# Kernel tuning notes

Hardware: AMD Instinct MI355X
Metric: run time of the kernel (lower is better)

The kernel has to match this reference:

```python
import jax, jax.numpy as jnp
import numpy as np

EMBED_DIM = 1024
LATEN_DIM = 1024
B, S = 4, 2048


def setup_inputs() -> dict:
    key = jax.random.key(0)
    k1, k2, k3, k4, k5 = jax.random.split(key, 5)
    xq = jax.random.normal(k1, (B, S, EMBED_DIM), dtype=jnp.float32)
    xk = jax.random.normal(k2, (B, S, EMBED_DIM), dtype=jnp.float32)
    xv = jax.random.normal(k3, (B, S, EMBED_DIM), dtype=jnp.float32)
    # Linear weight init similar to torch default scale
    bound = 1.0 / np.sqrt(EMBED_DIM)
    Wq = jax.random.uniform(k4, (EMBED_DIM, EMBED_DIM), minval=-bound, maxval=bound, dtype=jnp.float32)
    bq = jax.random.uniform(k5, (EMBED_DIM,), minval=-bound, maxval=bound, dtype=jnp.float32)
    # causal mask: 1 => masked (future positions)
    att_mask = jnp.triu(jnp.ones((S, S), dtype=jnp.int32), k=1)
    return {"xq": xq, "xk": xk, "xv": xv, "Wq": Wq, "bq": bq, "att_mask": att_mask}


def reference(xq, xk, xv, Wq, bq, att_mask):
    scale = LATEN_DIM ** (-0.5)
    # Faithful to source: linearQ is applied to all three inputs.
    Q = jnp.einsum('bsd,ed->bse', xq, Wq) + bq
    K = jnp.einsum('bsd,ed->bse', xk, Wq) + bq
    V = jnp.einsum('bsd,ed->bse', xv, Wq) + bq
    scores = jnp.einsum('bqe,bke->bqk', Q, K) * scale  # [B, S, S]
    scores = jnp.where(att_mask == 1, -jnp.inf, scores)
    probs = jax.nn.softmax(scores, axis=-1)
    return jnp.einsum('bqk,bke->bqe', probs, V)
```

## Files before the change

kernel.cpp:

```cpp
#include <hip/hip_runtime.h>
#include <hip/hip_bf16.h>
#include <stdint.h>


typedef __attribute__((ext_vector_type(8))) short bf16x8;
typedef __attribute__((ext_vector_type(4))) float floatx4;

#define DEVI static __device__ __forceinline__

static constexpr int S_ = 2048;
static constexpr int E_ = 1024;
static constexpr int BATCH = 4;
static constexpr int N4X = 8192 * 1024 / 4;

DEVI unsigned short f2b(float f) {
  union { float f; unsigned u; } v; v.f = f;
  return (unsigned short)((v.u + 0x7FFFu + ((v.u >> 16) & 1u)) >> 16);
}

DEVI void async_load16(const void* g, void* l) {
  __builtin_amdgcn_global_load_lds(
      (__attribute__((address_space(1))) void*)(void*)(g),
      (__attribute__((address_space(3))) void*)(l),
      16, 0, 0);
}

DEVI void mfma_tile(const unsigned short* lsA, const unsigned short* lsB,
                    int m0, int n0, int lrow, int lk, floatx4 (&acc)[4][4]) {
  bf16x8 af[4], bfr[4];
#pragma unroll
  for (int i = 0; i < 4; ++i)
    af[i] = *(const bf16x8*)(lsA + (m0 + i * 16 + lrow) * 32 + lk);
#pragma unroll
  for (int i = 0; i < 4; ++i)
    bfr[i] = *(const bf16x8*)(lsB + (n0 + i * 16 + lrow) * 32 + lk);
#pragma unroll
  for (int mi = 0; mi < 4; ++mi)
#pragma unroll
    for (int ni = 0; ni < 4; ++ni)
      acc[mi][ni] = __builtin_amdgcn_mfma_f32_16x16x32_bf16(
          af[mi], bfr[ni], acc[mi][ni], 0, 0, 0);
}

DEVI void stage_bf16(const unsigned short* src, unsigned short* ls, int ld,
                     int tid) {
#pragma unroll
  for (int j = 0; j < 2; ++j) {
    int t = tid + j * 256, row = t >> 2, kk = (t & 3) << 3;
    async_load16(src + (size_t)row * ld + kk, ls + t * 8);
  }
}

__global__ void cvt_all(const float* __restrict__ xq,
                        const float* __restrict__ xk,
                        const float* __restrict__ xv,
                        const float* __restrict__ Wq,
                        unsigned short* __restrict__ Xb,
                        unsigned short* __restrict__ Wb) {
  int i = blockIdx.x * blockDim.x + threadIdx.x;
  const float4* src;
  ushort4* dst;
  if (i < 3 * N4X) {
    int seg = i / N4X, off = i - seg * N4X;
    const float* s = (seg == 0) ? xq : (seg == 1) ? xk : xv;
    src = (const float4*)s + off;
    dst = (ushort4*)(Xb + (size_t)seg * 8192 * 1024) + off;
  } else {
    int off = i - 3 * N4X;
    src = (const float4*)Wq + off;
    dst = (ushort4*)Wb + off;
  }
  float4 v = *src;
  ushort4 o;
  o.x = f2b(v.x); o.y = f2b(v.y); o.z = f2b(v.z); o.w = f2b(v.w);
  *dst = o;
}

__global__ __launch_bounds__(256) void gemm_qkv(
    const unsigned short* __restrict__ Xb, const unsigned short* __restrict__ Wb,
    const float* __restrict__ bias, unsigned short* __restrict__ Qb,
    unsigned short* __restrict__ Kb, unsigned short* __restrict__ Vt) {
  __shared__ __align__(16) unsigned short lsA[2][128 * 32];
  __shared__ __align__(16) unsigned short lsB[2][128 * 32];
  const int l = blockIdx.x;
  const int xcd = l & 7, i = l >> 3;
  const int bn = i & 7;
  const int bmg = xcd * 24 + (i >> 3);
  const int input = bmg / 64, bm = bmg % 64;
  const unsigned short* A = Xb + (size_t)bmg * 128 * 1024;
  const unsigned short* W = Wb + (size_t)bn * 128 * 1024;

  const int tid = threadIdx.x;
  const int lane = tid & 63, wave = tid >> 6;
  const int m0 = (wave >> 1) * 64, n0 = (wave & 1) * 64;
  const int lrow = lane & 15, lk = (lane >> 4) * 8;

  floatx4 acc[4][4] = {};

  for (int kt = 0; kt < 16; ++kt) {
    if (kt) __syncthreads();
    stage_bf16(A + kt * 64, lsA[0], 1024, tid);
    stage_bf16(A + kt * 64 + 32, lsA[1], 1024, tid);
    stage_bf16(W + kt * 64, lsB[0], 1024, tid);
    stage_bf16(W + kt * 64 + 32, lsB[1], 1024, tid);
    __syncthreads();
    mfma_tile(lsA[0], lsB[0], m0, n0, lrow, lk, acc);
    mfma_tile(lsA[1], lsB[1], m0, n0, lrow, lk, acc);
  }

  unsigned short* C = (input == 0) ? Qb : (input == 1) ? Kb : Vt;
  const int rb = (lane >> 4) * 4;
#pragma unroll
  for (int mi = 0; mi < 4; ++mi)
#pragma unroll
    for (int ni = 0; ni < 4; ++ni) {
      int gcol = bn * 128 + n0 + ni * 16 + lrow;
      float bv = bias[gcol];
#pragma unroll
      for (int r = 0; r < 4; ++r) {
        int grow = bm * 128 + m0 + mi * 16 + rb + r;
        unsigned short val = f2b(acc[mi][ni][r] + bv);
        if (input == 2) {
          int b = grow >> 11, s = grow & 2047;
          C[((size_t)b * 1024 + gcol) * 2048 + s] = val;
        } else {
          C[(size_t)grow * 1024 + gcol] = val;
        }
      }
    }
}

__global__ __launch_bounds__(256) void gemm_scores_exp(
    const unsigned short* __restrict__ Qb,
    const unsigned short* __restrict__ Kb, unsigned short* __restrict__ P,
    float* __restrict__ lsum) {
  const int l = blockIdx.x;
  const int xcd = l & 7, k = l >> 3;
  const int m = k & 7, gl = k >> 3;
  const int gg = xcd * 12 + gl;
  const int z = gg / 24, r0 = gg % 24;
  const int bm = (r0 < 8) ? r0 : 8 + ((r0 - 8) >> 1);
  const int bn = ((r0 < 8) ? 0 : ((r0 - 8) & 1)) * 8 + m;
  if (bn > bm) return;

  __shared__ __align__(16) unsigned short lsA[2][128 * 32];
  __shared__ __align__(16) unsigned short lsB[2][128 * 32];
  const unsigned short* A = Qb + ((size_t)z * S_ + bm * 128) * E_;
  const unsigned short* Bt = Kb + ((size_t)z * S_ + bn * 128) * E_;
  const int tid = threadIdx.x;
  const int lane = tid & 63, wave = tid >> 6;
  const int m0 = (wave >> 1) * 64, n0 = (wave & 1) * 64;
  const int lrow = lane & 15, lk = (lane >> 4) * 8;

  floatx4 acc[4][4] = {};
  for (int kt = 0; kt < 16; ++kt) {
    if (kt) __syncthreads();
    stage_bf16(A + kt * 64, lsA[0], E_, tid);
    stage_bf16(A + kt * 64 + 32, lsA[1], E_, tid);
    stage_bf16(Bt + kt * 64, lsB[0], E_, tid);
    stage_bf16(Bt + kt * 64 + 32, lsB[1], E_, tid);
    __syncthreads();
    mfma_tile(lsA[0], lsB[0], m0, n0, lrow, lk, acc);
    mfma_tile(lsA[1], lsB[1], m0, n0, lrow, lk, acc);
  }

  const int rb = (lane >> 4) * 4;
  const bool diag = (bm == bn);
#pragma unroll
  for (int mi = 0; mi < 4; ++mi)
#pragma unroll
    for (int r = 0; r < 4; ++r) {
      const int grow = bm * 128 + m0 + mi * 16 + rb + r;
      float rsum = 0.f;
#pragma unroll
      for (int ni = 0; ni < 4; ++ni) {
        const int gcol = bn * 128 + n0 + ni * 16 + lrow;
        float p = __expf(acc[mi][ni][r] * 0.03125f);
        if (diag && gcol > grow) p = 0.f;
        P[((size_t)z * S_ + grow) * S_ + gcol] = f2b(p);
        rsum += p;
      }
#pragma unroll
      for (int off = 1; off < 16; off <<= 1) rsum += __shfl_xor(rsum, off);
      if ((lane & 15) == 0) atomicAdd(&lsum[z * S_ + grow], rsum);
    }
}

__global__ __launch_bounds__(256) void gemm_pv(
    const unsigned short* __restrict__ Pb,
    const unsigned short* __restrict__ Vt, const float* __restrict__ lsum,
    float* __restrict__ Out) {
  __shared__ __align__(16) unsigned short lsA[2][128 * 32];
  __shared__ __align__(16) unsigned short lsB[2][128 * 32];
  const int l = blockIdx.x;
  const int xcd = l & 7, i = l >> 3;
  const int bn = i & 7, j = i >> 3;
  const int z = j >> 1;
  const int bm = (j & 1) ? xcd : 15 - xcd;

  const unsigned short* A = Pb + ((size_t)z * S_ + bm * 128) * S_;
  const unsigned short* Bt = Vt + ((size_t)z * E_ + bn * 128) * S_;
  float* C = Out + (size_t)z * S_ * E_;
  const int tid = threadIdx.x;
  const int lane = tid & 63, wave = tid >> 6;
  const int m0 = (wave >> 1) * 64, n0 = (wave & 1) * 64;
  const int lrow = lane & 15, lk = (lane >> 4) * 8;

  floatx4 acc[4][4] = {};
  const int nKK = (bm + 1) * 2;
  for (int kt = 0; kt < nKK; ++kt) {
    if (kt) __syncthreads();
    stage_bf16(A + kt * 64, lsA[0], S_, tid);
    stage_bf16(A + kt * 64 + 32, lsA[1], S_, tid);
    stage_bf16(Bt + kt * 64, lsB[0], S_, tid);
    stage_bf16(Bt + kt * 64 + 32, lsB[1], S_, tid);
    __syncthreads();
    mfma_tile(lsA[0], lsB[0], m0, n0, lrow, lk, acc);
    mfma_tile(lsA[1], lsB[1], m0, n0, lrow, lk, acc);
  }

  const int rb = (lane >> 4) * 4;
#pragma unroll
  for (int mi = 0; mi < 4; ++mi)
#pragma unroll
    for (int r = 0; r < 4; ++r) {
      const int grow = bm * 128 + m0 + mi * 16 + rb + r;
      const float inv = 1.0f / lsum[z * S_ + grow];
#pragma unroll
      for (int ni = 0; ni < 4; ++ni) {
        const int gcol = bn * 128 + n0 + ni * 16 + lrow;
        C[(size_t)grow * E_ + gcol] = acc[mi][ni][r] * inv;
      }
    }
}

extern "C" void kernel_launch(void* const* d_in, const int* in_sizes, int n_in,
                              void* d_out, int out_size, void* d_ws,
                              size_t ws_size, hipStream_t stream) {
  (void)in_sizes; (void)n_in; (void)out_size; (void)ws_size;
  const float* xq = (const float*)d_in[0];
  const float* xk = (const float*)d_in[1];
  const float* xv = (const float*)d_in[2];
  const float* Wq = (const float*)d_in[3];
  const float* bq = (const float*)d_in[4];
  float* out = (float*)d_out;

  unsigned short* base16 = (unsigned short*)d_ws;
  unsigned short* Xb = base16;
  unsigned short* P = base16;
  unsigned short* Wb = base16 + (size_t)24 * 1024 * 1024;
  unsigned short* Qb = Wb + (size_t)1024 * 1024;
  unsigned short* Kb = Qb + (size_t)8192 * 1024;
  unsigned short* Vt = Kb + (size_t)8192 * 1024;
  float* lsum = (float*)(Vt + (size_t)8192 * 1024);

  hipMemsetAsync(lsum, 0, BATCH * S_ * sizeof(float), stream);

  const int n4tot = 3 * N4X + 1024 * 1024 / 4;
  cvt_all<<<n4tot / 256, 256, 0, stream>>>(xq, xk, xv, Wq, Xb, Wb);

  gemm_qkv<<<1536, 256, 0, stream>>>(Xb, Wb, bq, Qb, Kb, Vt);
  gemm_scores_exp<<<768, 256, 0, stream>>>(Qb, Kb, P, lsum);
  gemm_pv<<<512, 256, 0, stream>>>(P, Vt, lsum, out);
}
```

Before: 308.3 us.

## Double-buffer GEMM k-loop with swizzled LDS and 512-thread 128x256 tiles

```diff
diff --git a/kernel.cpp b/kernel.cpp
--- a/kernel.cpp
+++ b/kernel.cpp
@@ -25,29 +25,84 @@
       16, 0, 0);
 }
 
-DEVI void mfma_tile(const unsigned short* lsA, const unsigned short* lsB,
-                    int m0, int n0, int lrow, int lk, floatx4 (&acc)[4][4]) {
-  bf16x8 af[4], bfr[4];
-#pragma unroll
-  for (int i = 0; i < 4; ++i)
-    af[i] = *(const bf16x8*)(lsA + (m0 + i * 16 + lrow) * 32 + lk);
-#pragma unroll
-  for (int i = 0; i < 4; ++i)
-    bfr[i] = *(const bf16x8*)(lsB + (n0 + i * 16 + lrow) * 32 + lk);
-#pragma unroll
-  for (int mi = 0; mi < 4; ++mi)
-#pragma unroll
-    for (int ni = 0; ni < 4; ++ni)
-      acc[mi][ni] = __builtin_amdgcn_mfma_f32_16x16x32_bf16(
-          af[mi], bfr[ni], acc[mi][ni], 0, 0, 0);
-}
-
-DEVI void stage_bf16(const unsigned short* src, unsigned short* ls, int ld,
-                     int tid) {
-#pragma unroll
-  for (int j = 0; j < 2; ++j) {
-    int t = tid + j * 256, row = t >> 2, kk = (t & 3) << 3;
-    async_load16(src + (size_t)row * ld + kk, ls + t * 8);
+template <int ROWS>
+DEVI void stage(const unsigned short* __restrict__ src, int ld,
+                unsigned short* ls, int tid) {
+#pragma unroll
+  for (int j = 0; j < ROWS / 64; ++j) {
+    const int u = tid + j * 512;
+    const int row = u >> 3, slot = u & 7;
+    async_load16(src + row * ld + ((slot ^ (row & 7)) << 3), ls + u * 8);
+  }
+}
+
+DEVI bf16x8 ldfrag(const unsigned short* ls, int r, int kslot) {
+  return *(const bf16x8*)(ls + r * 64 + ((kslot ^ (r & 7)) << 3));
+}
+
+template <int NFR>
+DEVI void kloop(const unsigned short* __restrict__ A, int lda,
+                const unsigned short* __restrict__ Bm, int ldb, int NT,
+                unsigned short* lsA, unsigned short* lsB, int tid,
+                floatx4 (&acc)[4][NFR]) {
+  const int lane = tid & 63;
+  const int wr = (tid >> 6) >> 2, wc = (tid >> 6) & 3;
+  const int lrow = lane & 15, g = lane >> 4;
+  constexpr int BROWS = NFR * 64;
+  constexpr int AH = 128 * 64, BH = BROWS * 64;
+
+  stage<128>(A, lda, lsA, tid);
+  stage<BROWS>(Bm, ldb, lsB, tid);
+  if (NT > 1) {
+    stage<128>(A + 64, lda, lsA + AH, tid);
+    stage<BROWS>(Bm + 64, ldb, lsB + BH, tid);
+  }
+
+  for (int t = 0; t < NT; ++t) {
+    const int par = t & 1;
+    if (t + 1 < NT) {
+      if constexpr (NFR == 4)
+        asm volatile("s_waitcnt vmcnt(6)" ::: "memory");
+      else
+        asm volatile("s_waitcnt vmcnt(4)" ::: "memory");
+    } else {
+      asm volatile("s_waitcnt vmcnt(0)" ::: "memory");
+    }
+    asm volatile("s_barrier" ::: "memory");
+
+    const unsigned short* la = lsA + par * AH;
+    const unsigned short* lb = lsB + par * BH;
+    bf16x8 a[4][2];
+#pragma unroll
+    for (int mi = 0; mi < 4; ++mi)
+#pragma unroll
+      for (int ks = 0; ks < 2; ++ks)
+        a[mi][ks] = ldfrag(la, wr * 64 + mi * 16 + lrow, g + ks * 4);
+#pragma unroll
+    for (int nq = 0; nq < NFR / 2; ++nq) {
+      bf16x8 b[2][2];
+#pragma unroll
+      for (int ni = 0; ni < 2; ++ni)
+#pragma unroll
+        for (int ks = 0; ks < 2; ++ks)
+          b[ni][ks] = ldfrag(lb, wc * (NFR * 16) + (nq * 2 + ni) * 16 + lrow,
+                             g + ks * 4);
+      __builtin_amdgcn_s_setprio(1);
+#pragma unroll
+      for (int mi = 0; mi < 4; ++mi)
+#pragma unroll
+        for (int ni = 0; ni < 2; ++ni)
+#pragma unroll
+          for (int ks = 0; ks < 2; ++ks)
+            acc[mi][nq * 2 + ni] = __builtin_amdgcn_mfma_f32_16x16x32_bf16(
+                a[mi][ks], b[ni][ks], acc[mi][nq * 2 + ni], 0, 0, 0);
+      __builtin_amdgcn_s_setprio(0);
+    }
+    asm volatile("s_barrier" ::: "memory");
+    if (t + 2 < NT) {
+      stage<128>(A + (t + 2) * 64, lda, lsA + par * AH, tid);
+      stage<BROWS>(Bm + (t + 2) * 64, ldb, lsB + par * BH, tid);
+    }
   }
 }
 
@@ -76,50 +131,39 @@
   *dst = o;
 }
 
-__global__ __launch_bounds__(256) void gemm_qkv(
+__global__ __launch_bounds__(512) void gemm_qkv(
     const unsigned short* __restrict__ Xb, const unsigned short* __restrict__ Wb,
     const float* __restrict__ bias, unsigned short* __restrict__ Qb,
     unsigned short* __restrict__ Kb, unsigned short* __restrict__ Vt) {
-  __shared__ __align__(16) unsigned short lsA[2][128 * 32];
-  __shared__ __align__(16) unsigned short lsB[2][128 * 32];
+  __shared__ __align__(16) unsigned short lsA[2 * 128 * 64];
+  __shared__ __align__(16) unsigned short lsB[2 * 256 * 64];
   const int l = blockIdx.x;
   const int xcd = l & 7, i = l >> 3;
-  const int bn = i & 7;
-  const int bmg = xcd * 24 + (i >> 3);
-  const int input = bmg / 64, bm = bmg % 64;
+  const int gid = xcd * 96 + i;
+  const int bn = gid & 3, bmg = gid >> 2;
   const unsigned short* A = Xb + (size_t)bmg * 128 * 1024;
-  const unsigned short* W = Wb + (size_t)bn * 128 * 1024;
-
+  const unsigned short* W = Wb + (size_t)bn * 256 * 1024;
   const int tid = threadIdx.x;
+
+  floatx4 acc[4][4] = {};
+  kloop<4>(A, 1024, W, 1024, 16, lsA, lsB, tid, acc);
+
   const int lane = tid & 63, wave = tid >> 6;
-  const int m0 = (wave >> 1) * 64, n0 = (wave & 1) * 64;
-  const int lrow = lane & 15, lk = (lane >> 4) * 8;
-
-  floatx4 acc[4][4] = {};
-
-  for (int kt = 0; kt < 16; ++kt) {
-    if (kt) __syncthreads();
-    stage_bf16(A + kt * 64, lsA[0], 1024, tid);
-    stage_bf16(A + kt * 64 + 32, lsA[1], 1024, tid);
-    stage_bf16(W + kt * 64, lsB[0], 1024, tid);
-    stage_bf16(W + kt * 64 + 32, lsB[1], 1024, tid);
-    __syncthreads();
-    mfma_tile(lsA[0], lsB[0], m0, n0, lrow, lk, acc);
-    mfma_tile(lsA[1], lsB[1], m0, n0, lrow, lk, acc);
-  }
-
+  const int wr = wave >> 2, wc = wave & 3;
+  const int lrow = lane & 15, rb = (lane >> 4) * 4;
+  const int input = bmg >> 6;
   unsigned short* C = (input == 0) ? Qb : (input == 1) ? Kb : Vt;
-  const int rb = (lane >> 4) * 4;
+  const int rowbase = (bmg & 63) * 128 + wr * 64;
 #pragma unroll
   for (int mi = 0; mi < 4; ++mi)
 #pragma unroll
     for (int ni = 0; ni < 4; ++ni) {
-      int gcol = bn * 128 + n0 + ni * 16 + lrow;
-      float bv = bias[gcol];
+      const int gcol = bn * 256 + wc * 64 + ni * 16 + lrow;
+      const float bv = bias[gcol];
 #pragma unroll
       for (int r = 0; r < 4; ++r) {
-        int grow = bm * 128 + m0 + mi * 16 + rb + r;
-        unsigned short val = f2b(acc[mi][ni][r] + bv);
+        const int grow = rowbase + mi * 16 + rb + r;
+        const unsigned short val = f2b(acc[mi][ni][r] + bv);
         if (input == 2) {
           int b = grow >> 11, s = grow & 2047;
           C[((size_t)b * 1024 + gcol) * 2048 + s] = val;
@@ -130,51 +174,41 @@
     }
 }
 
-__global__ __launch_bounds__(256) void gemm_scores_exp(
+__global__ __launch_bounds__(512) void gemm_scores_exp(
     const unsigned short* __restrict__ Qb,
     const unsigned short* __restrict__ Kb, unsigned short* __restrict__ P,
     float* __restrict__ lsum) {
+  __shared__ __align__(16) unsigned short lsA[2 * 128 * 64];
+  __shared__ __align__(16) unsigned short lsB[2 * 256 * 64];
   const int l = blockIdx.x;
-  const int xcd = l & 7, k = l >> 3;
-  const int m = k & 7, gl = k >> 3;
-  const int gg = xcd * 12 + gl;
-  const int z = gg / 24, r0 = gg % 24;
-  const int bm = (r0 < 8) ? r0 : 8 + ((r0 - 8) >> 1);
-  const int bn = ((r0 < 8) ? 0 : ((r0 - 8) & 1)) * 8 + m;
-  if (bn > bm) return;
-
-  __shared__ __align__(16) unsigned short lsA[2][128 * 32];
-  __shared__ __align__(16) unsigned short lsB[2][128 * 32];
+  const int xcd = l & 7, i = l >> 3;
+  const int gid = xcd * 36 + i;
+  const int z = gid / 72;
+  int r0 = gid % 72;
+  int bm = 0;
+  for (;;) { const int c = (bm >> 1) + 1; if (r0 < c) break; r0 -= c; ++bm; }
+  const int bnn = r0;
+
   const unsigned short* A = Qb + ((size_t)z * S_ + bm * 128) * E_;
-  const unsigned short* Bt = Kb + ((size_t)z * S_ + bn * 128) * E_;
+  const unsigned short* Bt = Kb + ((size_t)z * S_ + bnn * 256) * E_;
   const int tid = threadIdx.x;
+
+  floatx4 acc[4][4] = {};
+  kloop<4>(A, E_, Bt, E_, 16, lsA, lsB, tid, acc);
+
   const int lane = tid & 63, wave = tid >> 6;
-  const int m0 = (wave >> 1) * 64, n0 = (wave & 1) * 64;
-  const int lrow = lane & 15, lk = (lane >> 4) * 8;
-
-  floatx4 acc[4][4] = {};
-  for (int kt = 0; kt < 16; ++kt) {
-    if (kt) __syncthreads();
-    stage_bf16(A + kt * 64, lsA[0], E_, tid);
-    stage_bf16(A + kt * 64 + 32, lsA[1], E_, tid);
-    stage_bf16(Bt + kt * 64, lsB[0], E_, tid);
-    stage_bf16(Bt + kt * 64 + 32, lsB[1], E_, tid);
-    __syncthreads();
-    mfma_tile(lsA[0], lsB[0], m0, n0, lrow, lk, acc);
-    mfma_tile(lsA[1], lsB[1], m0, n0, lrow, lk, acc);
-  }
-
-  const int rb = (lane >> 4) * 4;
-  const bool diag = (bm == bn);
+  const int wr = wave >> 2, wc = wave & 3;
+  const int lrow = lane & 15, rb = (lane >> 4) * 4;
+  const bool diag = (bnn == (bm >> 1));
 #pragma unroll
   for (int mi = 0; mi < 4; ++mi)
 #pragma unroll
     for (int r = 0; r < 4; ++r) {
-      const int grow = bm * 128 + m0 + mi * 16 + rb + r;
+      const int grow = bm * 128 + wr * 64 + mi * 16 + rb + r;
       float rsum = 0.f;
 #pragma unroll
       for (int ni = 0; ni < 4; ++ni) {
-        const int gcol = bn * 128 + n0 + ni * 16 + lrow;
+        const int gcol = bnn * 256 + wc * 64 + ni * 16 + lrow;
         float p = __expf(acc[mi][ni][r] * 0.03125f);
         if (diag && gcol > grow) p = 0.f;
         P[((size_t)z * S_ + grow) * S_ + gcol] = f2b(p);
@@ -186,12 +220,12 @@
     }
 }
 
-__global__ __launch_bounds__(256) void gemm_pv(
+__global__ __launch_bounds__(512) void gemm_pv(
     const unsigned short* __restrict__ Pb,
     const unsigned short* __restrict__ Vt, const float* __restrict__ lsum,
     float* __restrict__ Out) {
-  __shared__ __align__(16) unsigned short lsA[2][128 * 32];
-  __shared__ __align__(16) unsigned short lsB[2][128 * 32];
+  __shared__ __align__(16) unsigned short lsA[2 * 128 * 64];
+  __shared__ __align__(16) unsigned short lsB[2 * 128 * 64];
   const int l = blockIdx.x;
   const int xcd = l & 7, i = l >> 3;
   const int bn = i & 7, j = i >> 3;
@@ -202,33 +236,23 @@
   const unsigned short* Bt = Vt + ((size_t)z * E_ + bn * 128) * S_;
   float* C = Out + (size_t)z * S_ * E_;
   const int tid = threadIdx.x;
+  const int NT = 2 * bm + 2;
+
+  floatx4 acc[4][2] = {};
+  kloop<2>(A, S_, Bt, S_, NT, lsA, lsB, tid, acc);
+
   const int lane = tid & 63, wave = tid >> 6;
-  const int m0 = (wave >> 1) * 64, n0 = (wave & 1) * 64;
-  const int lrow = lane & 15, lk = (lane >> 4) * 8;
-
-  floatx4 acc[4][4] = {};
-  const int nKK = (bm + 1) * 2;
-  for (int kt = 0; kt < nKK; ++kt) {
-    if (kt) __syncthreads();
-    stage_bf16(A + kt * 64, lsA[0], S_, tid);
-    stage_bf16(A + kt * 64 + 32, lsA[1], S_, tid);
-    stage_bf16(Bt + kt * 64, lsB[0], S_, tid);
-    stage_bf16(Bt + kt * 64 + 32, lsB[1], S_, tid);
-    __syncthreads();
-    mfma_tile(lsA[0], lsB[0], m0, n0, lrow, lk, acc);
-    mfma_tile(lsA[1], lsB[1], m0, n0, lrow, lk, acc);
-  }
-
-  const int rb = (lane >> 4) * 4;
+  const int wr = wave >> 2, wc = wave & 3;
+  const int lrow = lane & 15, rb = (lane >> 4) * 4;
 #pragma unroll
   for (int mi = 0; mi < 4; ++mi)
 #pragma unroll
     for (int r = 0; r < 4; ++r) {
-      const int grow = bm * 128 + m0 + mi * 16 + rb + r;
+      const int grow = bm * 128 + wr * 64 + mi * 16 + rb + r;
       const float inv = 1.0f / lsum[z * S_ + grow];
 #pragma unroll
-      for (int ni = 0; ni < 4; ++ni) {
-        const int gcol = bn * 128 + n0 + ni * 16 + lrow;
+      for (int ni = 0; ni < 2; ++ni) {
+        const int gcol = bn * 128 + wc * 32 + ni * 16 + lrow;
         C[(size_t)grow * E_ + gcol] = acc[mi][ni][r] * inv;
       }
     }
@@ -259,7 +283,7 @@
   const int n4tot = 3 * N4X + 1024 * 1024 / 4;
   cvt_all<<<n4tot / 256, 256, 0, stream>>>(xq, xk, xv, Wq, Xb, Wb);
 
-  gemm_qkv<<<1536, 256, 0, stream>>>(Xb, Wb, bq, Qb, Kb, Vt);
-  gemm_scores_exp<<<768, 256, 0, stream>>>(Qb, Kb, P, lsum);
-  gemm_pv<<<512, 256, 0, stream>>>(P, Vt, lsum, out);
-}
+  gemm_qkv<<<768, 512, 0, stream>>>(Xb, Wb, bq, Qb, Kb, Vt);
+  gemm_scores_exp<<<288, 512, 0, stream>>>(Qb, Kb, P, lsum);
+  gemm_pv<<<512, 512, 0, stream>>>(P, Vt, lsum, out);
+}
```

Measured after the change: 336.7 us. 9.2% more time.

## Enlarge QKV GEMM tile to 256x128 with XOR-swizzled LDS layout

Applied to the files above, without the earlier changes.

```diff
diff --git a/kernel.cpp b/kernel.cpp
--- a/kernel.cpp
+++ b/kernel.cpp
@@ -25,6 +25,7 @@
       16, 0, 0);
 }
 
+
 DEVI void mfma_tile(const unsigned short* lsA, const unsigned short* lsB,
                     int m0, int n0, int lrow, int lk, floatx4 (&acc)[4][4]) {
   bf16x8 af[4], bfr[4];
@@ -49,6 +50,22 @@
     int t = tid + j * 256, row = t >> 2, kk = (t & 3) << 3;
     async_load16(src + (size_t)row * ld + kk, ls + t * 8);
   }
+}
+
+
+template <int ROWS, int NTHR>
+DEVI void stage_sw(const unsigned short* __restrict__ src, int ld,
+                   unsigned short* ls, int tid) {
+#pragma unroll
+  for (int j = 0; j < ROWS * 8 / NTHR; ++j) {
+    const int u = tid + j * NTHR;
+    const int row = u >> 3, slot = u & 7;
+    async_load16(src + row * ld + ((slot ^ (row & 7)) << 3), ls + u * 8);
+  }
+}
+
+DEVI bf16x8 ldfrag(const unsigned short* ls, int r, int kslot) {
+  return *(const bf16x8*)(ls + r * 64 + ((kslot ^ (r & 7)) << 3));
 }
 
 __global__ void cvt_all(const float* __restrict__ xq,
@@ -76,50 +93,61 @@
   *dst = o;
 }
 
-__global__ __launch_bounds__(256) void gemm_qkv(
+__global__ __launch_bounds__(256, 2) void gemm_qkv(
     const unsigned short* __restrict__ Xb, const unsigned short* __restrict__ Wb,
     const float* __restrict__ bias, unsigned short* __restrict__ Qb,
     unsigned short* __restrict__ Kb, unsigned short* __restrict__ Vt) {
-  __shared__ __align__(16) unsigned short lsA[2][128 * 32];
-  __shared__ __align__(16) unsigned short lsB[2][128 * 32];
+  __shared__ __align__(16) unsigned short lsA[256 * 64];
+  __shared__ __align__(16) unsigned short lsB[128 * 64];
   const int l = blockIdx.x;
   const int xcd = l & 7, i = l >> 3;
   const int bn = i & 7;
-  const int bmg = xcd * 24 + (i >> 3);
-  const int input = bmg / 64, bm = bmg % 64;
-  const unsigned short* A = Xb + (size_t)bmg * 128 * 1024;
+  const int bmg = xcd * 12 + (i >> 3);
+  const unsigned short* A = Xb + (size_t)bmg * 256 * 1024;
   const unsigned short* W = Wb + (size_t)bn * 128 * 1024;
-
   const int tid = threadIdx.x;
   const int lane = tid & 63, wave = tid >> 6;
-  const int m0 = (wave >> 1) * 64, n0 = (wave & 1) * 64;
-  const int lrow = lane & 15, lk = (lane >> 4) * 8;
-
-  floatx4 acc[4][4] = {};
-
+  const int wr = wave >> 1, wc = wave & 1;
+  const int lrow = lane & 15, g = lane >> 4;
+
+  floatx4 acc[8][4] = {};
   for (int kt = 0; kt < 16; ++kt) {
     if (kt) __syncthreads();
-    stage_bf16(A + kt * 64, lsA[0], 1024, tid);
-    stage_bf16(A + kt * 64 + 32, lsA[1], 1024, tid);
-    stage_bf16(W + kt * 64, lsB[0], 1024, tid);
-    stage_bf16(W + kt * 64 + 32, lsB[1], 1024, tid);
+    stage_sw<256, 256>(A + kt * 64, 1024, lsA, tid);
+    stage_sw<128, 256>(W + kt * 64, 1024, lsB, tid);
     __syncthreads();
-    mfma_tile(lsA[0], lsB[0], m0, n0, lrow, lk, acc);
-    mfma_tile(lsA[1], lsB[1], m0, n0, lrow, lk, acc);
-  }
-
+#pragma unroll
+    for (int ks = 0; ks < 2; ++ks) {
+      bf16x8 af[8], bfr[4];
+#pragma unroll
+      for (int mi = 0; mi < 8; ++mi)
+        af[mi] = ldfrag(lsA, wr * 128 + mi * 16 + lrow, ks * 4 + g);
+#pragma unroll
+      for (int ni = 0; ni < 4; ++ni)
+        bfr[ni] = ldfrag(lsB, wc * 64 + ni * 16 + lrow, ks * 4 + g);
+#pragma unroll
+      for (int mi = 0; mi < 8; ++mi)
+#pragma unroll
+        for (int ni = 0; ni < 4; ++ni)
+          acc[mi][ni] = __builtin_amdgcn_mfma_f32_16x16x32_bf16(
+              af[mi], bfr[ni], acc[mi][ni], 0, 0, 0);
+    }
+  }
+
+  const int rb = (lane >> 4) * 4;
+  const int input = bmg >> 5;
   unsigned short* C = (input == 0) ? Qb : (input == 1) ? Kb : Vt;
-  const int rb = (lane >> 4) * 4;
-#pragma unroll
-  for (int mi = 0; mi < 4; ++mi)
+  const int rowbase = (bmg & 31) * 256 + wr * 128;
+#pragma unroll
+  for (int mi = 0; mi < 8; ++mi)
 #pragma unroll
     for (int ni = 0; ni < 4; ++ni) {
-      int gcol = bn * 128 + n0 + ni * 16 + lrow;
-      float bv = bias[gcol];
+      const int gcol = bn * 128 + wc * 64 + ni * 16 + lrow;
+      const float bv = bias[gcol];
 #pragma unroll
       for (int r = 0; r < 4; ++r) {
-        int grow = bm * 128 + m0 + mi * 16 + rb + r;
-        unsigned short val = f2b(acc[mi][ni][r] + bv);
+        const int grow = rowbase + mi * 16 + rb + r;
+        const unsigned short val = f2b(acc[mi][ni][r] + bv);
         if (input == 2) {
           int b = grow >> 11, s = grow & 2047;
           C[((size_t)b * 1024 + gcol) * 2048 + s] = val;
@@ -259,7 +287,7 @@
   const int n4tot = 3 * N4X + 1024 * 1024 / 4;
   cvt_all<<<n4tot / 256, 256, 0, stream>>>(xq, xk, xv, Wq, Xb, Wb);
 
-  gemm_qkv<<<1536, 256, 0, stream>>>(Xb, Wb, bq, Qb, Kb, Vt);
+  gemm_qkv<<<768, 256, 0, stream>>>(Xb, Wb, bq, Qb, Kb, Vt);
   gemm_scores_exp<<<768, 256, 0, stream>>>(Qb, Kb, P, lsum);
   gemm_pv<<<512, 256, 0, stream>>>(P, Vt, lsum, out);
 }
```

After: 310.1 us. No clear change (+0.6%).

## Double-buffer LDS k-loop with async prefetch, XOR swizzle and MFMA priority

Applied to the files above, without the earlier changes.

```diff
diff --git a/kernel.cpp b/kernel.cpp
--- a/kernel.cpp
+++ b/kernel.cpp
@@ -25,29 +25,54 @@
       16, 0, 0);
 }
 
-DEVI void mfma_tile(const unsigned short* lsA, const unsigned short* lsB,
-                    int m0, int n0, int lrow, int lk, floatx4 (&acc)[4][4]) {
-  bf16x8 af[4], bfr[4];
-#pragma unroll
-  for (int i = 0; i < 4; ++i)
-    af[i] = *(const bf16x8*)(lsA + (m0 + i * 16 + lrow) * 32 + lk);
-#pragma unroll
-  for (int i = 0; i < 4; ++i)
-    bfr[i] = *(const bf16x8*)(lsB + (n0 + i * 16 + lrow) * 32 + lk);
-#pragma unroll
-  for (int mi = 0; mi < 4; ++mi)
-#pragma unroll
-    for (int ni = 0; ni < 4; ++ni)
-      acc[mi][ni] = __builtin_amdgcn_mfma_f32_16x16x32_bf16(
-          af[mi], bfr[ni], acc[mi][ni], 0, 0, 0);
-}
-
-DEVI void stage_bf16(const unsigned short* src, unsigned short* ls, int ld,
-                     int tid) {
+DEVI int swz(int row) { return (row & 3) ^ ((row >> 2) & 3); }
+
+DEVI void stage32(const unsigned short* __restrict__ src, unsigned short* ls,
+                  int ld, int tid) {
 #pragma unroll
   for (int j = 0; j < 2; ++j) {
-    int t = tid + j * 256, row = t >> 2, kk = (t & 3) << 3;
-    async_load16(src + (size_t)row * ld + kk, ls + t * 8);
+    int t = tid + j * 256, row = t >> 2, slot = t & 3;
+    async_load16(src + (size_t)row * ld + ((slot ^ swz(row)) << 3), ls + t * 8);
+  }
+}
+
+DEVI bf16x8 ldf(const unsigned short* ls, int r, int g) {
+  return *(const bf16x8*)(ls + r * 32 + ((g ^ swz(r)) << 3));
+}
+
+DEVI void kloop(const unsigned short* __restrict__ A, int lda,
+                const unsigned short* __restrict__ Bt, int ldb, int NT,
+                unsigned short* lsA0, unsigned short* lsA1,
+                unsigned short* lsB0, unsigned short* lsB1, int tid, int m0,
+                int n0, int lrow, int g, floatx4 (&acc)[4][4]) {
+  stage32(A, lsA0, lda, tid);
+  stage32(Bt, lsB0, ldb, tid);
+  for (int t = 0; t < NT; ++t) {
+    const int cur = t & 1;
+    unsigned short* la = cur ? lsA1 : lsA0;
+    unsigned short* lb = cur ? lsB1 : lsB0;
+    if (t + 1 < NT) {
+      stage32(A + (t + 1) * 32, cur ? lsA0 : lsA1, lda, tid);
+      stage32(Bt + (t + 1) * 32, cur ? lsB0 : lsB1, ldb, tid);
+      asm volatile("s_waitcnt vmcnt(4)" ::: "memory");
+    } else {
+      asm volatile("s_waitcnt vmcnt(0)" ::: "memory");
+    }
+    asm volatile("s_barrier" ::: "memory");
+    bf16x8 af[4], bfr[4];
+#pragma unroll
+    for (int i = 0; i < 4; ++i) af[i] = ldf(la, m0 + i * 16 + lrow, g);
+#pragma unroll
+    for (int i = 0; i < 4; ++i) bfr[i] = ldf(lb, n0 + i * 16 + lrow, g);
+    __builtin_amdgcn_s_setprio(1);
+#pragma unroll
+    for (int mi = 0; mi < 4; ++mi)
+#pragma unroll
+      for (int ni = 0; ni < 4; ++ni)
+        acc[mi][ni] = __builtin_amdgcn_mfma_f32_16x16x32_bf16(
+            af[mi], bfr[ni], acc[mi][ni], 0, 0, 0);
+    __builtin_amdgcn_s_setprio(0);
+    if (t + 1 < NT) asm volatile("s_barrier" ::: "memory");
   }
 }
 
@@ -93,20 +118,11 @@
   const int tid = threadIdx.x;
   const int lane = tid & 63, wave = tid >> 6;
   const int m0 = (wave >> 1) * 64, n0 = (wave & 1) * 64;
-  const int lrow = lane & 15, lk = (lane >> 4) * 8;
+  const int lrow = lane & 15, g = lane >> 4;
 
   floatx4 acc[4][4] = {};
-
-  for (int kt = 0; kt < 16; ++kt) {
-    if (kt) __syncthreads();
-    stage_bf16(A + kt * 64, lsA[0], 1024, tid);
-    stage_bf16(A + kt * 64 + 32, lsA[1], 1024, tid);
-    stage_bf16(W + kt * 64, lsB[0], 1024, tid);
-    stage_bf16(W + kt * 64 + 32, lsB[1], 1024, tid);
-    __syncthreads();
-    mfma_tile(lsA[0], lsB[0], m0, n0, lrow, lk, acc);
-    mfma_tile(lsA[1], lsB[1], m0, n0, lrow, lk, acc);
-  }
+  kloop(A, 1024, W, 1024, 32, lsA[0], lsA[1], lsB[0], lsB[1], tid, m0, n0,
+        lrow, g, acc);
 
   unsigned short* C = (input == 0) ? Qb : (input == 1) ? Kb : Vt;
   const int rb = (lane >> 4) * 4;
@@ -150,19 +166,11 @@
   const int tid = threadIdx.x;
   const int lane = tid & 63, wave = tid >> 6;
   const int m0 = (wave >> 1) * 64, n0 = (wave & 1) * 64;
-  const int lrow = lane & 15, lk = (lane >> 4) * 8;
+  const int lrow = lane & 15, g = lane >> 4;
 
   floatx4 acc[4][4] = {};
-  for (int kt = 0; kt < 16; ++kt) {
-    if (kt) __syncthreads();
-    stage_bf16(A + kt * 64, lsA[0], E_, tid);
-    stage_bf16(A + kt * 64 + 32, lsA[1], E_, tid);
-    stage_bf16(Bt + kt * 64, lsB[0], E_, tid);
-    stage_bf16(Bt + kt * 64 + 32, lsB[1], E_, tid);
-    __syncthreads();
-    mfma_tile(lsA[0], lsB[0], m0, n0, lrow, lk, acc);
-    mfma_tile(lsA[1], lsB[1], m0, n0, lrow, lk, acc);
-  }
+  kloop(A, E_, Bt, E_, 32, lsA[0], lsA[1], lsB[0], lsB[1], tid, m0, n0, lrow,
+        g, acc);
 
   const int rb = (lane >> 4) * 4;
   const bool diag = (bm == bn);
@@ -204,20 +212,12 @@
   const int tid = threadIdx.x;
   const int lane = tid & 63, wave = tid >> 6;
   const int m0 = (wave >> 1) * 64, n0 = (wave & 1) * 64;
-  const int lrow = lane & 15, lk = (lane >> 4) * 8;
+  const int lrow = lane & 15, g = lane >> 4;
 
   floatx4 acc[4][4] = {};
-  const int nKK = (bm + 1) * 2;
-  for (int kt = 0; kt < nKK; ++kt) {
-    if (kt) __syncthreads();
-    stage_bf16(A + kt * 64, lsA[0], S_, tid);
-    stage_bf16(A + kt * 64 + 32, lsA[1], S_, tid);
-    stage_bf16(Bt + kt * 64, lsB[0], S_, tid);
-    stage_bf16(Bt + kt * 64 + 32, lsB[1], S_, tid);
-    __syncthreads();
-    mfma_tile(lsA[0], lsB[0], m0, n0, lrow, lk, acc);
-    mfma_tile(lsA[1], lsB[1], m0, n0, lrow, lk, acc);
-  }
+  const int NT = (bm + 1) * 4;
+  kloop(A, S_, Bt, S_, NT, lsA[0], lsA[1], lsB[0], lsB[1], tid, m0, n0, lrow,
+        g, acc);
 
   const int rb = (lane >> 4) * 4;
 #pragma unroll
```

New measurement: 331.2 us. 7.4% more time.
